# Kernel optimization log

Hardware: AMD Instinct MI355X
Metric: run time of the kernel (lower is better)

Reference implementation:

```python
import jax, jax.numpy as jnp
import numpy as np

SIZES = [64, 64, 64, 64]
N_SAMPLES = 8192


def radialkernel(u, v):
    # exp(u.v^T - |u|^2/2 - |v|^2/2), shape [rows(u), rows(v)]
    uu = jnp.sum(u * u, axis=1, keepdims=True)
    vv = jnp.sum(v * v, axis=1, keepdims=True)
    return jnp.exp(u @ v.T - uu / 2 - vv.T / 2)


def setup_inputs() -> dict:
    key = jax.random.key(0)
    k0, k1, k2, k3 = jax.random.split(key, 4)
    d_in = 256
    total = sum(SIZES)            # 256
    rest = sum(SIZES[1:])         # 192
    data = jax.random.normal(k0, (N_SAMPLES, d_in), jnp.float32)
    inputs = jax.random.normal(k1, (2048, d_in), jnp.float32)
    # Linear(d_in, total): weight [total, d_in], bias [total]
    W = jax.random.normal(k2, (total, d_in), jnp.float32) / np.sqrt(d_in)
    b = jnp.zeros((total,), jnp.float32)
    # xavier_uniform for c_ss [N, rest]
    limit = np.sqrt(6.0 / (N_SAMPLES + rest)).astype(np.float32)
    c_ss = jax.random.uniform(k3, (N_SAMPLES, rest), jnp.float32, -limit, limit)
    return {"data": data, "inputs": inputs, "W": W, "b": b, "c_ss": c_ss}


def reference(data, inputs, W, b, c_ss):
    n = N_SAMPLES
    x = jnp.concatenate([data, inputs], axis=0) @ W.T + b  # [N+B, total]
    reg = jnp.sum(W * W) + jnp.sum(b * b)
    xss = list(jnp.split(x, np.cumsum(SIZES[:-1]), axis=1))
    css = jnp.split(c_ss, np.cumsum(SIZES[1:-1]), axis=1)
    ker = jnp.zeros((x.shape[0], n), x.dtype)
    for i, cs in enumerate(css):  # len(sizes)-1 iterations (small, fixed)
        xs = xss[i]
        ker = ker + radialkernel(xs, xs[:n])  # [N+B, N]
        val = ker @ cs                        # [N+B, sizes[i+1]]
        xss[i + 1] = xss[i + 1] + val
        reg = reg + jnp.sum(cs * val[:n])
    return xss[-1][n:], reg
```

## Files before the change

kernel.cpp:

```cpp
#include <hip/hip_runtime.h>
#include <hip/hip_bf16.h>

typedef unsigned short u16;
typedef unsigned int   u32;
typedef __attribute__((ext_vector_type(8)))  short bf16x8;
typedef __attribute__((ext_vector_type(16))) float f32x16;

#define N_S   8192
#define M_TOT 10240
#define SEGS  8
#define SEG   1024
#define QT    320

__device__ __forceinline__ u16 f2bf(float f) {
  u32 x = __float_as_uint(f);
  u32 r = x + 0x7FFFu + ((x >> 16) & 1u);
  return (u16)(r >> 16);
}
__device__ __forceinline__ float bf2f(u16 h) {
  return __uint_as_float(((u32)h) << 16);
}

__global__ __launch_bounds__(256) void gemm_x(const float* __restrict__ data,
                                              const float* __restrict__ inp,
                                              const float* __restrict__ W,
                                              const float* __restrict__ bias,
                                              float* __restrict__ x,
                                              u16* __restrict__ xb0,
                                              u32* __restrict__ hl0)
{
  __shared__ __align__(16) u16 At[64 * 256];
  __shared__ __align__(16) u16 Wt[64 * 256];
  __shared__ float part[64][2];
  const int t  = threadIdx.x;
  const int rb = blockIdx.x * 64, cb = blockIdx.y * 64;

#pragma unroll
  for (int it = 0; it < 8; ++it) {
    int c = it * 256 + t;
    int row = c >> 5, c8 = c & 31;
    int grow = rb + row;
    const float* src = (grow < N_S) ? data + (size_t)grow * 256 + c8 * 8
                                    : inp + (size_t)(grow - N_S) * 256 + c8 * 8;
    float4 v0 = *(const float4*)src;
    float4 v1 = *(const float4*)(src + 4);
    u16 h[8] = {f2bf(v0.x), f2bf(v0.y), f2bf(v0.z), f2bf(v0.w),
                f2bf(v1.x), f2bf(v1.y), f2bf(v1.z), f2bf(v1.w)};
    *(int4*)((char*)At + row * 512 + ((c8 * 16) ^ ((row & 7) << 4))) = *(int4*)h;

    const float* wsrc = W + (size_t)(cb + row) * 256 + c8 * 8;
    float4 w0 = *(const float4*)wsrc;
    float4 w1 = *(const float4*)(wsrc + 4);
    u16 g[8] = {f2bf(w0.x), f2bf(w0.y), f2bf(w0.z), f2bf(w0.w),
                f2bf(w1.x), f2bf(w1.y), f2bf(w1.z), f2bf(w1.w)};
    *(int4*)((char*)Wt + row * 512 + ((c8 * 16) ^ ((row & 7) << 4))) = *(int4*)g;
  }
  __syncthreads();

  const int w = t >> 6, lane = t & 63, l31 = lane & 31, hi = lane >> 5;
  const int wr = (w >> 1) * 32, wc = (w & 1) * 32;
  f32x16 acc;
#pragma unroll
  for (int r = 0; r < 16; ++r) acc[r] = 0.f;
  const char* Ab = (const char*)At + (size_t)(wr + l31) * 512;
  const char* Bb = (const char*)Wt + (size_t)(wc + l31) * 512;
  const int rx = (l31 & 7) << 4;
#pragma unroll
  for (int k0 = 0; k0 < 256; k0 += 16) {
    bf16x8 af = *(const bf16x8*)(Ab + ((k0 * 2 + hi * 16) ^ rx));
    bf16x8 bfv = *(const bf16x8*)(Bb + ((k0 * 2 + hi * 16) ^ rx));
    acc = __builtin_amdgcn_mfma_f32_32x32x16_bf16(af, bfv, acc, 0, 0, 0);
  }
  float bv = bias[cb + wc + l31];
#pragma unroll
  for (int r = 0; r < 16; ++r) {
    int qr = (r & 3) + 8 * (r >> 2) + 4 * hi;
    x[(size_t)(rb + wr + qr) * 256 + cb + wc + l31] = acc[r] + bv;
  }

  if (cb == 0) {
#pragma unroll
    for (int r = 0; r < 16; ++r) {
      int qr = (r & 3) + 8 * (r >> 2) + 4 * hi;
      u16 h = f2bf(acc[r] + bv);
      xb0[(size_t)(rb + wr + qr) * 64 + wc + l31] = h;
      float fb = bf2f(h);
      float s = fb * fb;
      s += __shfl_xor(s, 1);
      s += __shfl_xor(s, 2);
      s += __shfl_xor(s, 4);
      s += __shfl_xor(s, 8);
      s += __shfl_xor(s, 16);
      if (l31 == 0) part[wr + qr][w & 1] = s;
    }
    __syncthreads();
    if (t < 64) {
      float A = 0.5f * (part[t][0] + part[t][1]);
      u16 hq = f2bf(A);
      u16 lq = f2bf(A - bf2f(hq));
      hl0[rb + t] = (u32)hq | ((u32)lq << 16);
    }
  }
}

__global__ __launch_bounds__(256) void prep_csT(const float* __restrict__ css,
                                                u16* __restrict__ csbT)
{
  __shared__ float tile[64][65];
  const int i  = blockIdx.y;
  const int r0 = blockIdx.x * 64;
  const int t  = threadIdx.x;
#pragma unroll
  for (int it = 0; it < 4; ++it) {
    int r  = (t >> 4) + it * 16;
    int c4 = (t & 15) * 4;
    float4 v = *(const float4*)(css + (size_t)(r0 + r) * 192 + i * 64 + c4);
    tile[r][c4] = v.x; tile[r][c4 + 1] = v.y; tile[r][c4 + 2] = v.z; tile[r][c4 + 3] = v.w;
  }
  __syncthreads();
  const int c = t >> 2, rq = (t & 3) * 16;
  u16 tmp[16];
#pragma unroll
  for (int e = 0; e < 16; ++e) tmp[e] = f2bf(tile[rq + e][c]);
  u16* dst = csbT + (size_t)i * (64 * (size_t)N_S) + (size_t)c * N_S + r0 + rq;
  *(int4*)dst       = *(int4*)tmp;
  *(int4*)(dst + 8) = *(int4*)(tmp + 8);
}

__global__ __launch_bounds__(256) void regw_ker(const float* __restrict__ W,
                                                const float* __restrict__ bias,
                                                float* __restrict__ regpart,
                                                u32* __restrict__ mask)
{
  __shared__ float red[256];
  const int t = threadIdx.x, b = blockIdx.x;
  const int gid = b * 256 + t;
  if (gid < 3 * QT * SEGS) mask[gid] = 0u;
  float4 v = *(const float4*)(W + (size_t)b * 1024 + t * 4);
  float s = v.x * v.x + v.y * v.y + v.z * v.z + v.w * v.w;
  if (b == 0) { float bv = bias[t]; s += bv * bv; }
  red[t] = s; __syncthreads();
#pragma unroll
  for (int o = 128; o; o >>= 1) {
    if (t < o) red[t] += red[t + o];
    __syncthreads();
  }
  if (t == 0) regpart[b] = red[0];
}

__global__ __launch_bounds__(64) void screen_ker(const u16* __restrict__ xbj,
                                                 const u32* __restrict__ hlj,
                                                 u32* __restrict__ maskj)
{
  const int lane = threadIdx.x & 63, l31 = lane & 31, hi = lane >> 5;
  const int qq  = blockIdx.x;
  const int seg = blockIdx.y;
  const int w   = blockIdx.z;

  bf16x8 qf[4][4];
  u32 hlq[4];
#pragma unroll
  for (int q = 0; q < 4; ++q) {
    const int qrow = (qq * 4 + q) * 32 + l31;
    const u16* qp = xbj + (size_t)qrow * 64 + hi * 8;
#pragma unroll
    for (int d = 0; d < 4; ++d) qf[q][d] = *(const bf16x8*)(qp + d * 16);
    hlq[q] = hlj[qrow];
  }

  f32x16 Z;
#pragma unroll
  for (int r = 0; r < 16; ++r) Z[r] = 0.f;

  u32 bits[4] = {0u, 0u, 0u, 0u};
  const int nt0 = seg * 32 + w * 4;
#pragma unroll
  for (int it = 0; it < 4; ++it) {
    const int nb = (nt0 + it) * 32;
    const u16* kp = xbj + (size_t)(nb + l31) * 64 + hi * 8;
    bf16x8 kf0 = *(const bf16x8*)(kp);
    bf16x8 kf1 = *(const bf16x8*)(kp + 16);
    bf16x8 kf2 = *(const bf16x8*)(kp + 32);
    bf16x8 kf3 = *(const bf16x8*)(kp + 48);
    u32 hlk = hlj[nb + l31];
    union { bf16x8 v; u32 d[4]; } ke;
    ke.d[0] = hi ? 0u : 0xBF80BF80u;
    ke.d[1] = hi ? 0u : (hlk ^ 0x80008000u);
    ke.d[2] = 0u; ke.d[3] = 0u;
#pragma unroll
    for (int q = 0; q < 4; ++q) {
      f32x16 S = __builtin_amdgcn_mfma_f32_32x32x16_bf16(qf[q][0], kf0, Z, 0, 0, 0);
      S = __builtin_amdgcn_mfma_f32_32x32x16_bf16(qf[q][1], kf1, S, 0, 0, 0);
      S = __builtin_amdgcn_mfma_f32_32x32x16_bf16(qf[q][2], kf2, S, 0, 0, 0);
      S = __builtin_amdgcn_mfma_f32_32x32x16_bf16(qf[q][3], kf3, S, 0, 0, 0);
      union { bf16x8 v; u32 d[4]; } qe;
      qe.d[0] = hi ? 0u : hlq[q];
      qe.d[1] = hi ? 0u : 0x3F803F80u;
      qe.d[2] = 0u; qe.d[3] = 0u;
      S = __builtin_amdgcn_mfma_f32_32x32x16_bf16(qe.v, ke.v, S, 0, 0, 0);
      float m0 = fmaxf(S[0], S[1]),  m1 = fmaxf(S[2], S[3]);
      float m2 = fmaxf(S[4], S[5]),  m3 = fmaxf(S[6], S[7]);
      float m4 = fmaxf(S[8], S[9]),  m5 = fmaxf(S[10], S[11]);
      float m6 = fmaxf(S[12], S[13]), m7 = fmaxf(S[14], S[15]);
      float mx = fmaxf(fmaxf(fmaxf(m0, m1), fmaxf(m2, m3)),
                       fmaxf(fmaxf(m4, m5), fmaxf(m6, m7)));
      bits[q] |= (__any(mx > -25.0f) ? 1u : 0u) << it;
    }
  }
  if (lane == 0) {
#pragma unroll
    for (int q = 0; q < 4; ++q)
      if (bits[q]) atomicOr(&maskj[(size_t)(qq * 4 + q) * SEGS + seg], bits[q] << (w * 4));
  }
}

template<int NJ>
__global__ __launch_bounds__(256) void fused_ker(const u16* __restrict__ xb,
                                                 const u32* __restrict__ hl,
                                                 const u16* __restrict__ csbT,
                                                 float* __restrict__ val,
                                                 const u32* __restrict__ mask)
{
  __shared__ __align__(16) u16 Pt[4][32 * 32];

  const int t    = threadIdx.x;
  const int w    = t >> 6;
  const int lane = t & 63;
  const int l31  = lane & 31;
  const int hi   = lane >> 5;
  const int seg   = blockIdx.y;
  const int qtile = blockIdx.x * 4 + w;
  const int qrow  = qtile * 32 + l31;

  u32 m[NJ];
  u32 uni = 0;
#pragma unroll
  for (int j = 0; j < NJ; ++j) {
    m[j] = mask[((size_t)j * QT + qtile) * SEGS + seg];
    uni |= m[j];
  }
  if (!uni) return;

  float* vout = val + (size_t)seg * ((size_t)M_TOT * 64);

  bf16x8 qf[NJ][4];
  u32    hlq[NJ];
#pragma unroll
  for (int j = 0; j < NJ; ++j) {
    const u16* xbj = xb + (size_t)j * ((size_t)M_TOT * 64);
#pragma unroll
    for (int dk = 0; dk < 4; ++dk)
      qf[j][dk] = *(const bf16x8*)(xbj + (size_t)qrow * 64 + dk * 16 + hi * 8);
    hlq[j] = hl[j * M_TOT + qrow];
  }

  f32x16 acc0, acc1;
#pragma unroll
  for (int r = 0; r < 16; ++r) { acc0[r] = 0.f; acc1[r] = 0.f; }
  const int nb0 = seg * SEG;

  u32 rem = uni;
  while (rem) {
    const int nt = __ffs(rem) - 1;
    rem &= rem - 1;
    const int nb = nb0 + nt * 32;
    f32x16 P;
#pragma unroll
    for (int r = 0; r < 16; ++r) P[r] = 0.f;
#pragma unroll
    for (int j = 0; j < NJ; ++j) {
      if ((m[j] >> nt) & 1u) {
        const u16* xbj = xb + (size_t)j * ((size_t)M_TOT * 64);
        const u16* kp = xbj + (size_t)(nb + l31) * 64 + hi * 8;
        bf16x8 kf0 = *(const bf16x8*)(kp);
        bf16x8 kf1 = *(const bf16x8*)(kp + 16);
        bf16x8 kf2 = *(const bf16x8*)(kp + 32);
        bf16x8 kf3 = *(const bf16x8*)(kp + 48);
        u32 hlk = hl[j * M_TOT + nb + l31];
        f32x16 S;
#pragma unroll
        for (int r = 0; r < 16; ++r) S[r] = 0.f;
        S = __builtin_amdgcn_mfma_f32_32x32x16_bf16(qf[j][0], kf0, S, 0, 0, 0);
        S = __builtin_amdgcn_mfma_f32_32x32x16_bf16(qf[j][1], kf1, S, 0, 0, 0);
        S = __builtin_amdgcn_mfma_f32_32x32x16_bf16(qf[j][2], kf2, S, 0, 0, 0);
        S = __builtin_amdgcn_mfma_f32_32x32x16_bf16(qf[j][3], kf3, S, 0, 0, 0);
        union { bf16x8 v; u32 d[4]; } qe, ke;
        qe.d[0] = hi ? 0u : hlq[j];
        qe.d[1] = hi ? 0u : 0x3F803F80u;
        qe.d[2] = 0u; qe.d[3] = 0u;
        ke.d[0] = hi ? 0u : 0xBF80BF80u;
        ke.d[1] = hi ? 0u : (hlk ^ 0x80008000u);
        ke.d[2] = 0u; ke.d[3] = 0u;
        S = __builtin_amdgcn_mfma_f32_32x32x16_bf16(qe.v, ke.v, S, 0, 0, 0);
#pragma unroll
        for (int r = 0; r < 16; ++r) P[r] += __expf(S[r]);
      }
    }
    char* pw = (char*)&Pt[w][0];
#pragma unroll
    for (int r = 0; r < 16; ++r) {
      int qr = (r & 3) + 8 * (r >> 2) + 4 * hi;
      *(u16*)(pw + qr * 64 + ((l31 * 2) ^ ((qr & 3) << 4))) = f2bf(P[r]);
    }
    asm volatile("s_waitcnt lgkmcnt(0)" ::: "memory");
    bf16x8 pa0 = *(const bf16x8*)(pw + l31 * 64 + ((0  + hi * 16) ^ ((l31 & 3) << 4)));
    bf16x8 pa1 = *(const bf16x8*)(pw + l31 * 64 + ((32 + hi * 16) ^ ((l31 & 3) << 4)));
    asm volatile("s_waitcnt lgkmcnt(0)" ::: "memory");
    bf16x8 v00 = *(const bf16x8*)(csbT + (size_t)l31 * N_S + nb + hi * 8);
    bf16x8 v01 = *(const bf16x8*)(csbT + (size_t)l31 * N_S + nb + 16 + hi * 8);
    bf16x8 v10 = *(const bf16x8*)(csbT + (size_t)(32 + l31) * N_S + nb + hi * 8);
    bf16x8 v11 = *(const bf16x8*)(csbT + (size_t)(32 + l31) * N_S + nb + 16 + hi * 8);
    acc0 = __builtin_amdgcn_mfma_f32_32x32x16_bf16(pa0, v00, acc0, 0, 0, 0);
    acc0 = __builtin_amdgcn_mfma_f32_32x32x16_bf16(pa1, v01, acc0, 0, 0, 0);
    acc1 = __builtin_amdgcn_mfma_f32_32x32x16_bf16(pa0, v10, acc1, 0, 0, 0);
    acc1 = __builtin_amdgcn_mfma_f32_32x32x16_bf16(pa1, v11, acc1, 0, 0, 0);
  }

#pragma unroll
  for (int r = 0; r < 16; ++r) {
    int qr = (r & 3) + 8 * (r >> 2) + 4 * hi;
    size_t row = (size_t)(qtile * 32 + qr);
    vout[row * 64 + l31]      = acc0[r];
    vout[row * 64 + 32 + l31] = acc1[r];
  }
}

__global__ __launch_bounds__(256) void apply_ker(const float* __restrict__ val,
                                                 const float* __restrict__ css,
                                                 float* __restrict__ x, int i, int nj,
                                                 const u32* __restrict__ mask,
                                                 float* __restrict__ dotpart,
                                                 u16* __restrict__ xbn,
                                                 u32* __restrict__ hln,
                                                 float* __restrict__ out)
{
  __shared__ float red[256];
  const int t = threadIdx.x;
  const int qtile = blockIdx.x;
  const int row = qtile * 32 + (t >> 3);
  const int coff = (t & 7) * 8;
  bool f[SEGS];
  bool anyf = false;
#pragma unroll
  for (int s = 0; s < SEGS; ++s) {
    u32 u = 0;
    for (int j = 0; j < nj; ++j) u |= mask[((size_t)j * QT + qtile) * SEGS + s];
    f[s] = (u != 0);
    anyf = anyf || f[s];
  }
  float v[8];
#pragma unroll
  for (int e = 0; e < 8; ++e) v[e] = 0.f;
  float dp = 0.f;
  float* xp = x + (size_t)row * 256 + (size_t)(i + 1) * 64 + coff;
  float4 xa = *(const float4*)xp;
  float4 xb4 = *(const float4*)(xp + 4);
  if (anyf) {
#pragma unroll
    for (int s = 0; s < SEGS; ++s) if (f[s]) {
      const float* vp = val + (size_t)s * ((size_t)M_TOT * 64) + (size_t)row * 64 + coff;
      float4 a = *(const float4*)vp;
      float4 b = *(const float4*)(vp + 4);
      v[0] += a.x; v[1] += a.y; v[2] += a.z; v[3] += a.w;
      v[4] += b.x; v[5] += b.y; v[6] += b.z; v[7] += b.w;
    }
    if (row < N_S) {
      const float* cp = css + (size_t)row * 192 + (size_t)i * 64 + coff;
      float4 ca = *(const float4*)cp;
      float4 cb = *(const float4*)(cp + 4);
      dp = ca.x * v[0] + ca.y * v[1] + ca.z * v[2] + ca.w * v[3]
         + cb.x * v[4] + cb.y * v[5] + cb.z * v[6] + cb.w * v[7];
    }
  }
  xa.x += v[0]; xa.y += v[1]; xa.z += v[2]; xa.w += v[3];
  xb4.x += v[4]; xb4.y += v[5]; xb4.z += v[6]; xb4.w += v[7];
  if (i < 2) {
    if (anyf) {
      *(float4*)xp = xa;
      *(float4*)(xp + 4) = xb4;
    }
  } else if (row >= N_S) {
    float* op = out + (size_t)(row - N_S) * 64 + coff;
    *(float4*)op = xa;
    *(float4*)(op + 4) = xb4;
  }
  if (xbn) {
    float xv[8] = {xa.x, xa.y, xa.z, xa.w, xb4.x, xb4.y, xb4.z, xb4.w};
    u16 h[8];
    float s2 = 0.f;
#pragma unroll
    for (int e = 0; e < 8; ++e) {
      h[e] = f2bf(xv[e]);
      float fb = bf2f(h[e]);
      s2 += fb * fb;
    }
    *(int4*)(xbn + (size_t)row * 64 + coff) = *(int4*)h;
    s2 += __shfl_xor(s2, 1);
    s2 += __shfl_xor(s2, 2);
    s2 += __shfl_xor(s2, 4);
    if ((t & 7) == 0) {
      float A = 0.5f * s2;
      u16 hq = f2bf(A);
      u16 lq = f2bf(A - bf2f(hq));
      hln[row] = (u32)hq | ((u32)lq << 16);
    }
  }
  red[t] = dp; __syncthreads();
#pragma unroll
  for (int o = 128; o; o >>= 1) {
    if (t < o) red[t] += red[t + o];
    __syncthreads();
  }
  if (t == 0) dotpart[i * QT + qtile] = red[0];
}

__global__ __launch_bounds__(256) void final_ker(const float* __restrict__ regpart,
                                                 const float* __restrict__ dotpart,
                                                 float* __restrict__ out)
{
  __shared__ float red[256];
  float s = 0.f;
  for (int idx = threadIdx.x; idx < 3 * QT; idx += 256) s += dotpart[idx];
  if (threadIdx.x < 64) s += regpart[threadIdx.x];
  red[threadIdx.x] = s; __syncthreads();
#pragma unroll
  for (int o = 128; o; o >>= 1) {
    if (threadIdx.x < o) red[threadIdx.x] += red[threadIdx.x + o];
    __syncthreads();
  }
  if (threadIdx.x == 0) out[131072] = red[0];
}

extern "C" void kernel_launch(void* const* d_in, const int* in_sizes, int n_in,
                              void* d_out, int out_size, void* d_ws, size_t ws_size,
                              hipStream_t stream)
{
  const float* data = (const float*)d_in[0];
  const float* inp  = (const float*)d_in[1];
  const float* W    = (const float*)d_in[2];
  const float* bias = (const float*)d_in[3];
  const float* css  = (const float*)d_in[4];
  float* out = (float*)d_out;

  char* ws = (char*)d_ws;
  const size_t OFF_X    = 0;
  const size_t OFF_XB   = 10485760;
  const size_t OFF_HL   = OFF_XB + 3932160;
  const size_t OFF_CSBT = OFF_HL + 122880;
  const size_t OFF_VAL  = OFF_CSBT + 3145728;
  const size_t OFF_MASK = OFF_VAL + 20971520;
  const size_t OFF_REGW = OFF_MASK + 30720;
  const size_t OFF_DOT  = OFF_REGW + 256;

  float* x      = (float*)(ws + OFF_X);
  u16*   xb     = (u16*)  (ws + OFF_XB);
  u32*   hl     = (u32*)  (ws + OFF_HL);
  u16*   csbT   = (u16*)  (ws + OFF_CSBT);
  float* val    = (float*)(ws + OFF_VAL);
  u32*   mask   = (u32*)  (ws + OFF_MASK);
  float* regpart= (float*)(ws + OFF_REGW);
  float* dotpart= (float*)(ws + OFF_DOT);

  const size_t XB_STRIDE = (size_t)M_TOT * 64;
  const size_t CS_STRIDE = (size_t)64 * N_S;
  const size_t MK_STRIDE = (size_t)QT * SEGS;

  gemm_x   <<<dim3(160, 4), 256, 0, stream>>>(data, inp, W, bias, x, xb, hl);
  prep_csT <<<dim3(128, 3), 256, 0, stream>>>(css, csbT);
  regw_ker <<<64, 256, 0, stream>>>(W, bias, regpart, mask);
  screen_ker<<<dim3(80, SEGS, 8), 64, 0, stream>>>(xb, hl, mask);

  fused_ker<1><<<dim3(80, SEGS), 256, 0, stream>>>(xb, hl, csbT, val, mask);
  apply_ker<<<QT, 256, 0, stream>>>(val, css, x, 0, 1, mask, dotpart,
                                    xb + XB_STRIDE, hl + M_TOT, (float*)nullptr);
  screen_ker<<<dim3(80, SEGS, 8), 64, 0, stream>>>(xb + XB_STRIDE, hl + M_TOT, mask + MK_STRIDE);

  fused_ker<2><<<dim3(80, SEGS), 256, 0, stream>>>(xb, hl, csbT + CS_STRIDE, val, mask);
  apply_ker<<<QT, 256, 0, stream>>>(val, css, x, 1, 2, mask, dotpart,
                                    xb + 2 * XB_STRIDE, hl + 2 * M_TOT, (float*)nullptr);
  screen_ker<<<dim3(80, SEGS, 8), 64, 0, stream>>>(xb + 2 * XB_STRIDE, hl + 2 * M_TOT, mask + 2 * MK_STRIDE);

  fused_ker<3><<<dim3(80, SEGS), 256, 0, stream>>>(xb, hl, csbT + 2 * CS_STRIDE, val, mask);
  apply_ker<<<QT, 256, 0, stream>>>(val, css, x, 2, 3, mask, dotpart,
                                    (u16*)nullptr, (u32*)nullptr, out);

  final_ker<<<1, 256, 0, stream>>>(regpart, dotpart, out);
}
```

Measured before the change: 152.7 us.

## Fuse kernel-matmul and apply stages, merge setup kernels, fold final reduction

Merges the csT transpose and W-norm/mask-clear kernels into one setup kernel, and fuses the per-segment fused kernel with the apply kernel. Each block now owns one 32-row query tile and spreads active 32-column key tiles across its four waves round-robin, reducing the partial results in shared memory instead of writing per-segment partials to a global val buffer and reading them back. The final scalar reduction is folded into the last fa_ker via an atomic counter, removing a launch. The trade-off is fewer blocks (320 instead of 640) with uneven work per block, and a larger shared-memory footprint that can lower occupancy.

```diff
diff --git a/kernel.cpp b/kernel.cpp
--- a/kernel.cpp
+++ b/kernel.cpp
@@ -103,49 +103,51 @@
   }
 }
 
-__global__ __launch_bounds__(256) void prep_csT(const float* __restrict__ css,
-                                                u16* __restrict__ csbT)
+__global__ __launch_bounds__(256) void setup_ker(const float* __restrict__ css,
+                                                 const float* __restrict__ W,
+                                                 const float* __restrict__ bias,
+                                                 u16* __restrict__ csbT,
+                                                 float* __restrict__ regpart,
+                                                 u32* __restrict__ mask,
+                                                 u32* __restrict__ counter)
 {
   __shared__ float tile[64][65];
-  const int i  = blockIdx.y;
-  const int r0 = blockIdx.x * 64;
-  const int t  = threadIdx.x;
-#pragma unroll
-  for (int it = 0; it < 4; ++it) {
-    int r  = (t >> 4) + it * 16;
-    int c4 = (t & 15) * 4;
-    float4 v = *(const float4*)(css + (size_t)(r0 + r) * 192 + i * 64 + c4);
-    tile[r][c4] = v.x; tile[r][c4 + 1] = v.y; tile[r][c4 + 2] = v.z; tile[r][c4 + 3] = v.w;
-  }
-  __syncthreads();
-  const int c = t >> 2, rq = (t & 3) * 16;
-  u16 tmp[16];
-#pragma unroll
-  for (int e = 0; e < 16; ++e) tmp[e] = f2bf(tile[rq + e][c]);
-  u16* dst = csbT + (size_t)i * (64 * (size_t)N_S) + (size_t)c * N_S + r0 + rq;
-  *(int4*)dst       = *(int4*)tmp;
-  *(int4*)(dst + 8) = *(int4*)(tmp + 8);
-}
-
-__global__ __launch_bounds__(256) void regw_ker(const float* __restrict__ W,
-                                                const float* __restrict__ bias,
-                                                float* __restrict__ regpart,
-                                                u32* __restrict__ mask)
-{
   __shared__ float red[256];
-  const int t = threadIdx.x, b = blockIdx.x;
-  const int gid = b * 256 + t;
-  if (gid < 3 * QT * SEGS) mask[gid] = 0u;
-  float4 v = *(const float4*)(W + (size_t)b * 1024 + t * 4);
-  float s = v.x * v.x + v.y * v.y + v.z * v.z + v.w * v.w;
-  if (b == 0) { float bv = bias[t]; s += bv * bv; }
-  red[t] = s; __syncthreads();
-#pragma unroll
-  for (int o = 128; o; o >>= 1) {
-    if (t < o) red[t] += red[t + o];
+  const int b = blockIdx.x, t = threadIdx.x;
+  if (b < 384) {
+    const int i  = b >> 7;
+    const int r0 = (b & 127) * 64;
+#pragma unroll
+    for (int it = 0; it < 4; ++it) {
+      int r  = (t >> 4) + it * 16;
+      int c4 = (t & 15) * 4;
+      float4 v = *(const float4*)(css + (size_t)(r0 + r) * 192 + i * 64 + c4);
+      tile[r][c4] = v.x; tile[r][c4 + 1] = v.y; tile[r][c4 + 2] = v.z; tile[r][c4 + 3] = v.w;
+    }
     __syncthreads();
-  }
-  if (t == 0) regpart[b] = red[0];
+    const int c = t >> 2, rq = (t & 3) * 16;
+    u16 tmp[16];
+#pragma unroll
+    for (int e = 0; e < 16; ++e) tmp[e] = f2bf(tile[rq + e][c]);
+    u16* dst = csbT + (size_t)i * (64 * (size_t)N_S) + (size_t)c * N_S + r0 + rq;
+    *(int4*)dst       = *(int4*)tmp;
+    *(int4*)(dst + 8) = *(int4*)(tmp + 8);
+  } else {
+    const int b2 = b - 384;
+    const int gid = b2 * 256 + t;
+    if (gid < 3 * QT * SEGS) mask[gid] = 0u;
+    if (gid == 0) *counter = 0u;
+    float4 v = *(const float4*)(W + (size_t)b2 * 1024 + t * 4);
+    float s = v.x * v.x + v.y * v.y + v.z * v.z + v.w * v.w;
+    if (b2 == 0) { float bv = bias[t]; s += bv * bv; }
+    red[t] = s; __syncthreads();
+#pragma unroll
+    for (int o = 128; o; o >>= 1) {
+      if (t < o) red[t] += red[t + o];
+      __syncthreads();
+    }
+    if (t == 0) regpart[b2] = red[0];
+  }
 }
 
 __global__ __launch_bounds__(64) void screen_ker(const u16* __restrict__ xbj,
@@ -215,33 +217,32 @@
 }
 
 template<int NJ>
-__global__ __launch_bounds__(256) void fused_ker(const u16* __restrict__ xb,
-                                                 const u32* __restrict__ hl,
-                                                 const u16* __restrict__ csbT,
-                                                 float* __restrict__ val,
-                                                 const u32* __restrict__ mask)
+__global__ __launch_bounds__(256) void fa_ker(const u16* __restrict__ xb,
+                                              const u32* __restrict__ hl,
+                                              const u16* __restrict__ csbT,
+                                              const u32* __restrict__ mask,
+                                              const float* __restrict__ css,
+                                              float* __restrict__ x,
+                                              float* __restrict__ dotpart,
+                                              u16* __restrict__ xbn,
+                                              u32* __restrict__ hln,
+                                              float* __restrict__ out,
+                                              const float* __restrict__ regpart,
+                                              u32* __restrict__ counter)
 {
   __shared__ __align__(16) u16 Pt[4][32 * 32];
+  __shared__ float accs[4][32][64];
+  __shared__ float red[256];
+  __shared__ int lastFlag;
 
   const int t    = threadIdx.x;
   const int w    = t >> 6;
   const int lane = t & 63;
   const int l31  = lane & 31;
   const int hi   = lane >> 5;
-  const int seg   = blockIdx.y;
-  const int qtile = blockIdx.x * 4 + w;
+  const int qtile = blockIdx.x;
   const int qrow  = qtile * 32 + l31;
-
-  u32 m[NJ];
-  u32 uni = 0;
-#pragma unroll
-  for (int j = 0; j < NJ; ++j) {
-    m[j] = mask[((size_t)j * QT + qtile) * SEGS + seg];
-    uni |= m[j];
-  }
-  if (!uni) return;
-
-  float* vout = val + (size_t)seg * ((size_t)M_TOT * 64);
+  constexpr int I = NJ - 1;
 
   bf16x8 qf[NJ][4];
   u32    hlq[NJ];
@@ -257,134 +258,109 @@
   f32x16 acc0, acc1;
 #pragma unroll
   for (int r = 0; r < 16; ++r) { acc0[r] = 0.f; acc1[r] = 0.f; }
-  const int nb0 = seg * SEG;
-
-  u32 rem = uni;
-  while (rem) {
-    const int nt = __ffs(rem) - 1;
-    rem &= rem - 1;
-    const int nb = nb0 + nt * 32;
-    f32x16 P;
-#pragma unroll
-    for (int r = 0; r < 16; ++r) P[r] = 0.f;
+
+  int idx = 0;
+  for (int seg = 0; seg < SEGS; ++seg) {
+    u32 mj[NJ];
+    u32 uni = 0;
 #pragma unroll
     for (int j = 0; j < NJ; ++j) {
-      if ((m[j] >> nt) & 1u) {
-        const u16* xbj = xb + (size_t)j * ((size_t)M_TOT * 64);
-        const u16* kp = xbj + (size_t)(nb + l31) * 64 + hi * 8;
-        bf16x8 kf0 = *(const bf16x8*)(kp);
-        bf16x8 kf1 = *(const bf16x8*)(kp + 16);
-        bf16x8 kf2 = *(const bf16x8*)(kp + 32);
-        bf16x8 kf3 = *(const bf16x8*)(kp + 48);
-        u32 hlk = hl[j * M_TOT + nb + l31];
-        f32x16 S;
-#pragma unroll
-        for (int r = 0; r < 16; ++r) S[r] = 0.f;
-        S = __builtin_amdgcn_mfma_f32_32x32x16_bf16(qf[j][0], kf0, S, 0, 0, 0);
-        S = __builtin_amdgcn_mfma_f32_32x32x16_bf16(qf[j][1], kf1, S, 0, 0, 0);
-        S = __builtin_amdgcn_mfma_f32_32x32x16_bf16(qf[j][2], kf2, S, 0, 0, 0);
-        S = __builtin_amdgcn_mfma_f32_32x32x16_bf16(qf[j][3], kf3, S, 0, 0, 0);
-        union { bf16x8 v; u32 d[4]; } qe, ke;
-        qe.d[0] = hi ? 0u : hlq[j];
-        qe.d[1] = hi ? 0u : 0x3F803F80u;
-        qe.d[2] = 0u; qe.d[3] = 0u;
-        ke.d[0] = hi ? 0u : 0xBF80BF80u;
-        ke.d[1] = hi ? 0u : (hlk ^ 0x80008000u);
-        ke.d[2] = 0u; ke.d[3] = 0u;
-        S = __builtin_amdgcn_mfma_f32_32x32x16_bf16(qe.v, ke.v, S, 0, 0, 0);
-#pragma unroll
-        for (int r = 0; r < 16; ++r) P[r] += __expf(S[r]);
+      mj[j] = mask[((size_t)j * QT + qtile) * SEGS + seg];
+      uni |= mj[j];
+    }
+    u32 rem = uni;
+    while (rem) {
+      const int nt = __ffs(rem) - 1;
+      rem &= rem - 1;
+      if ((idx++ & 3) != w) continue;
+      const int nb = seg * SEG + nt * 32;
+      f32x16 P;
+#pragma unroll
+      for (int r = 0; r < 16; ++r) P[r] = 0.f;
+#pragma unroll
+      for (int j = 0; j < NJ; ++j) {
+        if ((mj[j] >> nt) & 1u) {
+          const u16* xbj = xb + (size_t)j * ((size_t)M_TOT * 64);
+          const u16* kp = xbj + (size_t)(nb + l31) * 64 + hi * 8;
+          bf16x8 kf0 = *(const bf16x8*)(kp);
+          bf16x8 kf1 = *(const bf16x8*)(kp + 16);
+          bf16x8 kf2 = *(const bf16x8*)(kp + 32);
+          bf16x8 kf3 = *(const bf16x8*)(kp + 48);
+          u32 hlk = hl[j * M_TOT + nb + l31];
+          f32x16 S;
+#pragma unroll
+          for (int r = 0; r < 16; ++r) S[r] = 0.f;
+          S = __builtin_amdgcn_mfma_f32_32x32x16_bf16(qf[j][0], kf0, S, 0, 0, 0);
+          S = __builtin_amdgcn_mfma_f32_32x32x16_bf16(qf[j][1], kf1, S, 0, 0, 0);
+          S = __builtin_amdgcn_mfma_f32_32x32x16_bf16(qf[j][2], kf2, S, 0, 0, 0);
+          S = __builtin_amdgcn_mfma_f32_32x32x16_bf16(qf[j][3], kf3, S, 0, 0, 0);
+          union { bf16x8 v; u32 d[4]; } qe, ke;
+          qe.d[0] = hi ? 0u : hlq[j];
+          qe.d[1] = hi ? 0u : 0x3F803F80u;
+          qe.d[2] = 0u; qe.d[3] = 0u;
+          ke.d[0] = hi ? 0u : 0xBF80BF80u;
+          ke.d[1] = hi ? 0u : (hlk ^ 0x80008000u);
+          ke.d[2] = 0u; ke.d[3] = 0u;
+          S = __builtin_amdgcn_mfma_f32_32x32x16_bf16(qe.v, ke.v, S, 0, 0, 0);
+#pragma unroll
+          for (int r = 0; r < 16; ++r) P[r] += __expf(S[r]);
+        }
       }
-    }
-    char* pw = (char*)&Pt[w][0];
-#pragma unroll
-    for (int r = 0; r < 16; ++r) {
-      int qr = (r & 3) + 8 * (r >> 2) + 4 * hi;
-      *(u16*)(pw + qr * 64 + ((l31 * 2) ^ ((qr & 3) << 4))) = f2bf(P[r]);
-    }
-    asm volatile("s_waitcnt lgkmcnt(0)" ::: "memory");
-    bf16x8 pa0 = *(const bf16x8*)(pw + l31 * 64 + ((0  + hi * 16) ^ ((l31 & 3) << 4)));
-    bf16x8 pa1 = *(const bf16x8*)(pw + l31 * 64 + ((32 + hi * 16) ^ ((l31 & 3) << 4)));
-    asm volatile("s_waitcnt lgkmcnt(0)" ::: "memory");
-    bf16x8 v00 = *(const bf16x8*)(csbT + (size_t)l31 * N_S + nb + hi * 8);
-    bf16x8 v01 = *(const bf16x8*)(csbT + (size_t)l31 * N_S + nb + 16 + hi * 8);
-    bf16x8 v10 = *(const bf16x8*)(csbT + (size_t)(32 + l31) * N_S + nb + hi * 8);
-    bf16x8 v11 = *(const bf16x8*)(csbT + (size_t)(32 + l31) * N_S + nb + 16 + hi * 8);
-    acc0 = __builtin_amdgcn_mfma_f32_32x32x16_bf16(pa0, v00, acc0, 0, 0, 0);
-    acc0 = __builtin_amdgcn_mfma_f32_32x32x16_bf16(pa1, v01, acc0, 0, 0, 0);
-    acc1 = __builtin_amdgcn_mfma_f32_32x32x16_bf16(pa0, v10, acc1, 0, 0, 0);
-    acc1 = __builtin_amdgcn_mfma_f32_32x32x16_bf16(pa1, v11, acc1, 0, 0, 0);
+      char* pw = (char*)&Pt[w][0];
+#pragma unroll
+      for (int r = 0; r < 16; ++r) {
+        int qr = (r & 3) + 8 * (r >> 2) + 4 * hi;
+        *(u16*)(pw + qr * 64 + ((l31 * 2) ^ ((qr & 3) << 4))) = f2bf(P[r]);
+      }
+      asm volatile("s_waitcnt lgkmcnt(0)" ::: "memory");
+      bf16x8 pa0 = *(const bf16x8*)(pw + l31 * 64 + ((0  + hi * 16) ^ ((l31 & 3) << 4)));
+      bf16x8 pa1 = *(const bf16x8*)(pw + l31 * 64 + ((32 + hi * 16) ^ ((l31 & 3) << 4)));
+      asm volatile("s_waitcnt lgkmcnt(0)" ::: "memory");
+      bf16x8 v00 = *(const bf16x8*)(csbT + (size_t)l31 * N_S + nb + hi * 8);
+      bf16x8 v01 = *(const bf16x8*)(csbT + (size_t)l31 * N_S + nb + 16 + hi * 8);
+      bf16x8 v10 = *(const bf16x8*)(csbT + (size_t)(32 + l31) * N_S + nb + hi * 8);
+      bf16x8 v11 = *(const bf16x8*)(csbT + (size_t)(32 + l31) * N_S + nb + 16 + hi * 8);
+      acc0 = __builtin_amdgcn_mfma_f32_32x32x16_bf16(pa0, v00, acc0, 0, 0, 0);
+      acc0 = __builtin_amdgcn_mfma_f32_32x32x16_bf16(pa1, v01, acc0, 0, 0, 0);
+      acc1 = __builtin_amdgcn_mfma_f32_32x32x16_bf16(pa0, v10, acc1, 0, 0, 0);
+      acc1 = __builtin_amdgcn_mfma_f32_32x32x16_bf16(pa1, v11, acc1, 0, 0, 0);
+    }
   }
 
 #pragma unroll
   for (int r = 0; r < 16; ++r) {
     int qr = (r & 3) + 8 * (r >> 2) + 4 * hi;
-    size_t row = (size_t)(qtile * 32 + qr);
-    vout[row * 64 + l31]      = acc0[r];
-    vout[row * 64 + 32 + l31] = acc1[r];
-  }
-}
-
-__global__ __launch_bounds__(256) void apply_ker(const float* __restrict__ val,
-                                                 const float* __restrict__ css,
-                                                 float* __restrict__ x, int i, int nj,
-                                                 const u32* __restrict__ mask,
-                                                 float* __restrict__ dotpart,
-                                                 u16* __restrict__ xbn,
-                                                 u32* __restrict__ hln,
-                                                 float* __restrict__ out)
-{
-  __shared__ float red[256];
-  const int t = threadIdx.x;
-  const int qtile = blockIdx.x;
-  const int row = qtile * 32 + (t >> 3);
+    accs[w][qr][l31]      = acc0[r];
+    accs[w][qr][32 + l31] = acc1[r];
+  }
+  __syncthreads();
+
+  const int rr   = t >> 3;
+  const int row  = qtile * 32 + rr;
   const int coff = (t & 7) * 8;
-  bool f[SEGS];
-  bool anyf = false;
-#pragma unroll
-  for (int s = 0; s < SEGS; ++s) {
-    u32 u = 0;
-    for (int j = 0; j < nj; ++j) u |= mask[((size_t)j * QT + qtile) * SEGS + s];
-    f[s] = (u != 0);
-    anyf = anyf || f[s];
-  }
   float v[8];
 #pragma unroll
-  for (int e = 0; e < 8; ++e) v[e] = 0.f;
+  for (int e = 0; e < 8; ++e)
+    v[e] = ((accs[0][rr][coff + e] + accs[1][rr][coff + e]) +
+            (accs[2][rr][coff + e] + accs[3][rr][coff + e]));
+
   float dp = 0.f;
-  float* xp = x + (size_t)row * 256 + (size_t)(i + 1) * 64 + coff;
-  float4 xa = *(const float4*)xp;
-  float4 xb4 = *(const float4*)(xp + 4);
-  if (anyf) {
-#pragma unroll
-    for (int s = 0; s < SEGS; ++s) if (f[s]) {
-      const float* vp = val + (size_t)s * ((size_t)M_TOT * 64) + (size_t)row * 64 + coff;
-      float4 a = *(const float4*)vp;
-      float4 b = *(const float4*)(vp + 4);
-      v[0] += a.x; v[1] += a.y; v[2] += a.z; v[3] += a.w;
-      v[4] += b.x; v[5] += b.y; v[6] += b.z; v[7] += b.w;
-    }
-    if (row < N_S) {
-      const float* cp = css + (size_t)row * 192 + (size_t)i * 64 + coff;
-      float4 ca = *(const float4*)cp;
-      float4 cb = *(const float4*)(cp + 4);
-      dp = ca.x * v[0] + ca.y * v[1] + ca.z * v[2] + ca.w * v[3]
-         + cb.x * v[4] + cb.y * v[5] + cb.z * v[6] + cb.w * v[7];
-    }
-  }
-  xa.x += v[0]; xa.y += v[1]; xa.z += v[2]; xa.w += v[3];
-  xb4.x += v[4]; xb4.y += v[5]; xb4.z += v[6]; xb4.w += v[7];
-  if (i < 2) {
-    if (anyf) {
-      *(float4*)xp = xa;
-      *(float4*)(xp + 4) = xb4;
-    }
-  } else if (row >= N_S) {
-    float* op = out + (size_t)(row - N_S) * 64 + coff;
-    *(float4*)op = xa;
-    *(float4*)(op + 4) = xb4;
-  }
-  if (xbn) {
+  if (row < N_S) {
+    const float* cp = css + (size_t)row * 192 + (size_t)I * 64 + coff;
+    float4 ca = *(const float4*)cp;
+    float4 cb = *(const float4*)(cp + 4);
+    dp = ca.x * v[0] + ca.y * v[1] + ca.z * v[2] + ca.w * v[3]
+       + cb.x * v[4] + cb.y * v[5] + cb.z * v[6] + cb.w * v[7];
+  }
+
+  if (NJ < 3) {
+    float* xp = x + (size_t)row * 256 + (size_t)(I + 1) * 64 + coff;
+    float4 xa = *(const float4*)xp;
+    float4 xb4 = *(const float4*)(xp + 4);
+    xa.x += v[0]; xa.y += v[1]; xa.z += v[2]; xa.w += v[3];
+    xb4.x += v[4]; xb4.y += v[5]; xb4.z += v[6]; xb4.w += v[7];
+    *(float4*)xp = xa;
+    *(float4*)(xp + 4) = xb4;
     float xv[8] = {xa.x, xa.y, xa.z, xa.w, xb4.x, xb4.y, xb4.z, xb4.w};
     u16 h[8];
     float s2 = 0.f;
@@ -404,31 +380,44 @@
       u16 lq = f2bf(A - bf2f(hq));
       hln[row] = (u32)hq | ((u32)lq << 16);
     }
-  }
+  } else if (row >= N_S) {
+    const float* xp = x + (size_t)row * 256 + 192 + coff;
+    float4 xa = *(const float4*)xp;
+    float4 xb4 = *(const float4*)(xp + 4);
+    float* op = out + (size_t)(row - N_S) * 64 + coff;
+    float4 oa = {xa.x + v[0], xa.y + v[1], xa.z + v[2], xa.w + v[3]};
+    float4 ob = {xb4.x + v[4], xb4.y + v[5], xb4.z + v[6], xb4.w + v[7]};
+    *(float4*)op = oa;
+    *(float4*)(op + 4) = ob;
+  }
+
   red[t] = dp; __syncthreads();
 #pragma unroll
   for (int o = 128; o; o >>= 1) {
     if (t < o) red[t] += red[t + o];
     __syncthreads();
   }
-  if (t == 0) dotpart[i * QT + qtile] = red[0];
-}
-
-__global__ __launch_bounds__(256) void final_ker(const float* __restrict__ regpart,
-                                                 const float* __restrict__ dotpart,
-                                                 float* __restrict__ out)
-{
-  __shared__ float red[256];
-  float s = 0.f;
-  for (int idx = threadIdx.x; idx < 3 * QT; idx += 256) s += dotpart[idx];
-  if (threadIdx.x < 64) s += regpart[threadIdx.x];
-  red[threadIdx.x] = s; __syncthreads();
-#pragma unroll
-  for (int o = 128; o; o >>= 1) {
-    if (threadIdx.x < o) red[threadIdx.x] += red[threadIdx.x + o];
+  if (t == 0) dotpart[I * QT + qtile] = red[0];
+
+  if (NJ == 3) {
+    if (t == 0) {
+      u32 c = __hip_atomic_fetch_add(counter, 1u, __ATOMIC_ACQ_REL, __HIP_MEMORY_SCOPE_AGENT);
+      lastFlag = (c == QT - 1) ? 1 : 0;
+    }
     __syncthreads();
-  }
-  if (threadIdx.x == 0) out[131072] = red[0];
+    if (lastFlag) {
+      float s = 0.f;
+      for (int i2 = t; i2 < 3 * QT; i2 += 256) s += dotpart[i2];
+      if (t < 64) s += regpart[t];
+      red[t] = s; __syncthreads();
+#pragma unroll
+      for (int o = 128; o; o >>= 1) {
+        if (t < o) red[t] += red[t + o];
+        __syncthreads();
+      }
+      if (t == 0) out[131072] = red[0];
+    }
+  }
 }
 
 extern "C" void kernel_launch(void* const* d_in, const int* in_sizes, int n_in,
@@ -447,42 +436,39 @@
   const size_t OFF_XB   = 10485760;
   const size_t OFF_HL   = OFF_XB + 3932160;
   const size_t OFF_CSBT = OFF_HL + 122880;
-  const size_t OFF_VAL  = OFF_CSBT + 3145728;
-  const size_t OFF_MASK = OFF_VAL + 20971520;
+  const size_t OFF_MASK = OFF_CSBT + 3145728;
   const size_t OFF_REGW = OFF_MASK + 30720;
   const size_t OFF_DOT  = OFF_REGW + 256;
+  const size_t OFF_CNT  = OFF_DOT + 3840;
 
   float* x      = (float*)(ws + OFF_X);
   u16*   xb     = (u16*)  (ws + OFF_XB);
   u32*   hl     = (u32*)  (ws + OFF_HL);
   u16*   csbT   = (u16*)  (ws + OFF_CSBT);
-  float* val    = (float*)(ws + OFF_VAL);
   u32*   mask   = (u32*)  (ws + OFF_MASK);
   float* regpart= (float*)(ws + OFF_REGW);
   float* dotpart= (float*)(ws + OFF_DOT);
+  u32*   counter= (u32*)  (ws + OFF_CNT);
 
   const size_t XB_STRIDE = (size_t)M_TOT * 64;
   const size_t CS_STRIDE = (size_t)64 * N_S;
   const size_t MK_STRIDE = (size_t)QT * SEGS;
 
+  setup_ker<<<448, 256, 0, stream>>>(css, W, bias, csbT, regpart, mask, counter);
   gemm_x   <<<dim3(160, 4), 256, 0, stream>>>(data, inp, W, bias, x, xb, hl);
-  prep_csT <<<dim3(128, 3), 256, 0, stream>>>(css, csbT);
-  regw_ker <<<64, 256, 0, stream>>>(W, bias, regpart, mask);
   screen_ker<<<dim3(80, SEGS, 8), 64, 0, stream>>>(xb, hl, mask);
 
-  fused_ker<1><<<dim3(80, SEGS), 256, 0, stream>>>(xb, hl, csbT, val, mask);
-  apply_ker<<<QT, 256, 0, stream>>>(val, css, x, 0, 1, mask, dotpart,
-                                    xb + XB_STRIDE, hl + M_TOT, (float*)nullptr);
+  fa_ker<1><<<QT, 256, 0, stream>>>(xb, hl, csbT, mask, css, x, dotpart,
+                                    xb + XB_STRIDE, hl + M_TOT, (float*)nullptr,
+                                    regpart, counter);
   screen_ker<<<dim3(80, SEGS, 8), 64, 0, stream>>>(xb + XB_STRIDE, hl + M_TOT, mask + MK_STRIDE);
 
-  fused_ker<2><<<dim3(80, SEGS), 256, 0, stream>>>(xb, hl, csbT + CS_STRIDE, val, mask);
-  apply_ker<<<QT, 256, 0, stream>>>(val, css, x, 1, 2, mask, dotpart,
-                                    xb + 2 * XB_STRIDE, hl + 2 * M_TOT, (float*)nullptr);
+  fa_ker<2><<<QT, 256, 0, stream>>>(xb, hl, csbT + CS_STRIDE, mask, css, x, dotpart,
+                                    xb + 2 * XB_STRIDE, hl + 2 * M_TOT, (float*)nullptr,
+                                    regpart, counter);
   screen_ker<<<dim3(80, SEGS, 8), 64, 0, stream>>>(xb + 2 * XB_STRIDE, hl + 2 * M_TOT, mask + 2 * MK_STRIDE);
 
-  fused_ker<3><<<dim3(80, SEGS), 256, 0, stream>>>(xb, hl, csbT + 2 * CS_STRIDE, val, mask);
-  apply_ker<<<QT, 256, 0, stream>>>(val, css, x, 2, 3, mask, dotpart,
-                                    (u16*)nullptr, (u32*)nullptr, out);
-
-  final_ker<<<1, 256, 0, stream>>>(regpart, dotpart, out);
-}
+  fa_ker<3><<<QT, 256, 0, stream>>>(xb, hl, csbT + 2 * CS_STRIDE, mask, css, x, dotpart,
+                                    (u16*)nullptr, (u32*)nullptr, out,
+                                    regpart, counter);
+}
```

After: 149.4 us. 2.2% less time.
